# Kernel tuning notes

Hardware: AMD Instinct MI355X
Metric: run time of the kernel (lower is better)

The kernel has to match this reference:

```python
import jax, jax.numpy as jnp
import numpy as np

B, N, D, TOP_K = 4, 4096, 256, 64
EPS = 1e-12  # F.normalize default eps


def setup_inputs() -> dict:
    key = jax.random.key(0)
    kx, kw, kb = jax.random.split(key, 3)
    x = jax.random.normal(kx, (B, N, D), dtype=jnp.float32)
    # value_fc: nn.Linear(in_dims, in_dims) -> weight [D, D], bias [D]
    lim = 1.0 / np.sqrt(D)
    W = jax.random.uniform(kw, (D, D), dtype=jnp.float32, minval=-lim, maxval=lim)
    b = jax.random.uniform(kb, (D,), dtype=jnp.float32, minval=-lim, maxval=lim)
    return {"x": x, "W": W, "b": b}


def reference(x, W, b):
    # value = value_fc(x)
    value = jnp.einsum("bnd,ed->bne", x, W) + b  # torch Linear: x @ W.T + b
    # F.normalize(x, p=2, dim=-1)
    norm = jnp.linalg.norm(x, axis=-1, keepdims=True)
    normed_x = x / jnp.maximum(norm, EPS)
    # full cosine-similarity matrix [B, N, N]
    cos_sim = jnp.einsum("bnd,bmd->bnm", normed_x, normed_x)
    # topk along last dim, scatter back into zeros
    topk_vals, topk_inds = jax.lax.top_k(cos_sim, TOP_K)  # [B, N, K]
    b_idx = jnp.arange(x.shape[0])[:, None, None]
    n_idx = jnp.arange(x.shape[1])[None, :, None]
    attn_sparse = jnp.zeros_like(cos_sim).at[b_idx, n_idx, topk_inds].set(topk_vals)
    # softmax over full row (zeros at non-topk positions contribute exp(0))
    attn = jax.nn.softmax(attn_sparse, axis=-1)
    return jnp.einsum("bnm,bmd->bnd", attn, value)
```

## Files before the change

kernel.cpp:

```cpp
#include <hip/hip_runtime.h>
#include <hip/hip_bf16.h>
#include <stdint.h>

#define B_ 4
#define N_ 4096
#define D_ 256
#define K_ 64
#define BN_ (B_*N_)

typedef __attribute__((ext_vector_type(8))) short bf16x8;
typedef __attribute__((ext_vector_type(8))) unsigned short u16x8;
typedef __attribute__((ext_vector_type(4))) float f32x4;
typedef __attribute__((address_space(1))) const unsigned int gas_u32;
typedef __attribute__((address_space(3))) unsigned int las_u32;

static __device__ __forceinline__ unsigned short f2bf(float f) {
  union { float f; unsigned u; } x; x.f = f;
  unsigned r = x.u + 0x7fffu + ((x.u >> 16) & 1u);
  return (unsigned short)(r >> 16);
}
static __device__ __forceinline__ float bf2f(unsigned short u) {
  union { unsigned u; float f; } x; x.u = ((unsigned)u) << 16;
  return x.f;
}
static __device__ __forceinline__ f32x4 mfma16(bf16x8 a, bf16x8 b, f32x4 c) {
  return __builtin_amdgcn_mfma_f32_16x16x32_bf16(a, b, c, 0, 0, 0);
}

__global__ __launch_bounds__(256) void prep_kernel(
    const float* __restrict__ x, const float* __restrict__ W,
    unsigned short* __restrict__ xn, float* __restrict__ norms,
    unsigned short* __restrict__ Wb, float* __restrict__ vsum) {
  const int bid = blockIdx.x;
  if (bid < 4096) {
    int row = bid * 4 + (threadIdx.x >> 6);
    int lane = threadIdx.x & 63;
    const float4 v = reinterpret_cast<const float4*>(x + (size_t)row * D_)[lane];
    float ss = v.x*v.x + v.y*v.y + v.z*v.z + v.w*v.w;
    #pragma unroll
    for (int off = 32; off > 0; off >>= 1) ss += __shfl_xor(ss, off);
    float nrm = sqrtf(ss);
    float scale = 1.0f / fmaxf(nrm, 1e-12f);
    ushort4 o;
    o.x = f2bf(v.x * scale); o.y = f2bf(v.y * scale);
    o.z = f2bf(v.z * scale); o.w = f2bf(v.w * scale);
    reinterpret_cast<ushort4*>(xn + (size_t)row * D_)[lane] = o;
    if (lane == 0) norms[row] = nrm;
  } else if (bid < 4160) {
    int i = (bid - 4096) * 256 + threadIdx.x;
    float4 v = reinterpret_cast<const float4*>(W)[i];
    ushort4 o; o.x = f2bf(v.x); o.y = f2bf(v.y); o.z = f2bf(v.z); o.w = f2bf(v.w);
    reinterpret_cast<ushort4*>(Wb)[i] = o;
  } else {
    reinterpret_cast<float4*>(vsum)[threadIdx.x] = (float4){0.f, 0.f, 0.f, 0.f};
  }
}

__global__ __launch_bounds__(256, 3) void compute_kernel(
    const unsigned short* __restrict__ xn, const float* __restrict__ norms,
    const unsigned short* __restrict__ Wb, const float* __restrict__ bias,
    unsigned short* __restrict__ value, float* __restrict__ vsum,
    unsigned short* __restrict__ S) {
  __shared__ __attribute__((aligned(16))) unsigned char smem[33792];
  unsigned char* As = smem;
  unsigned char* Bs = smem + 16384;
  float* ns_s   = (float*)(smem + 32768);
  float* bias_s = (float*)(smem + 33280);

  const int t = threadIdx.x, lane = t & 63, w = t >> 6;
  const int l15 = lane & 15, qv = lane >> 4, rb = qv * 4;
  const int wr = w >> 1, wc = w & 1;
  const int x7 = l15 & 7;

  const unsigned short* Asrc;
  const unsigned short* Bsrc;
  int rbG, cb, batch = 0;
  const bool vmode = (blockIdx.x < 256);
  if (vmode) {
    rbG = (blockIdx.x >> 1) * 128;
    cb  = (blockIdx.x & 1) * 128;
    Asrc = xn + (size_t)rbG * D_;
    Bsrc = Wb + (size_t)cb * D_;
    if (t < 128) { ns_s[t] = norms[rbG + t]; bias_s[t] = bias[cb + t]; }
  } else {
    int g = blockIdx.x - 256;
    batch = g >> 10;
    int tl = g & 1023;
    rbG = (tl >> 5) * 128;
    cb  = (tl & 31) * 128;
    Asrc = xn + ((size_t)batch * N_ + rbG) * D_;
    Bsrc = xn + ((size_t)batch * N_ + cb)  * D_;
  }

  auto STAGE = [&](int kk) {
    #pragma unroll
    for (int p = 0; p < 4; p++) {
      int q = t + p * 256;
      int row = q >> 3, c = q & 7;
      int cg = (c ^ (row & 7)) * 8;
      __builtin_amdgcn_global_load_lds(
          (gas_u32*)(Asrc + (size_t)row * D_ + kk * 64 + cg),
          (las_u32*)(As + q * 16), 16, 0, 0);
      __builtin_amdgcn_global_load_lds(
          (gas_u32*)(Bsrc + (size_t)row * D_ + kk * 64 + cg),
          (las_u32*)(Bs + q * 16), 16, 0, 0);
    }
  };

  f32x4 acc[4][4];
  #pragma unroll
  for (int i = 0; i < 4; i++)
    #pragma unroll
    for (int j = 0; j < 4; j++) acc[i][j] = (f32x4){0.f,0.f,0.f,0.f};

  STAGE(0);
  __syncthreads();
  for (int kk = 0; kk < 4; kk++) {
    bf16x8 afr[2][4], bfr[2][4];
    #pragma unroll
    for (int ks = 0; ks < 2; ks++) {
      const int cpos = (((ks * 4 + qv) ^ x7) << 4);
      #pragma unroll
      for (int rt = 0; rt < 4; rt++)
        afr[ks][rt] = *(const bf16x8*)(As + (wr*64 + rt*16 + l15) * 128 + cpos);
      #pragma unroll
      for (int ct = 0; ct < 4; ct++)
        bfr[ks][ct] = *(const bf16x8*)(Bs + (wc*64 + ct*16 + l15) * 128 + cpos);
    }
    __syncthreads();
    if (kk < 3) STAGE(kk + 1);
    #pragma unroll
    for (int ks = 0; ks < 2; ks++)
      #pragma unroll
      for (int rt = 0; rt < 4; rt++)
        #pragma unroll
        for (int ct = 0; ct < 4; ct++)
          acc[rt][ct] = mfma16(afr[ks][rt], bfr[ks][ct], acc[rt][ct]);
    if (kk < 3) __syncthreads();
  }

  unsigned short* kbuf = (unsigned short*)smem;
  if (vmode) {
    float vpart[4] = {0.f, 0.f, 0.f, 0.f};
    #pragma unroll
    for (int rt = 0; rt < 4; rt++)
      #pragma unroll
      for (int ct = 0; ct < 4; ct++) {
        int col_l = wc*64 + ct*16 + l15;
        #pragma unroll
        for (int reg = 0; reg < 4; reg++) {
          int row_l = wr*64 + rt*16 + rb + reg;
          float v = acc[rt][ct][reg] * ns_s[row_l] + bias_s[col_l];
          int pos = (col_l & 7) | ((((col_l >> 3) ^ (row_l & 7))) << 3);
          kbuf[row_l * 128 + pos] = f2bf(v);
          vpart[ct] += v;
        }
      }
    int b2 = rbG >> 12;
    #pragma unroll
    for (int ct = 0; ct < 4; ct++)
      atomicAdd(&vsum[b2*D_ + cb + wc*64 + ct*16 + l15], vpart[ct]);
    __syncthreads();
    #pragma unroll
    for (int p = 0; p < 8; p++) {
      int q = t + p * 256;
      int row = q >> 4, c8 = q & 15;
      u16x8 d = *(const u16x8*)(kbuf + row * 128 + ((c8 ^ (row & 7)) << 3));
      *(u16x8*)(value + (size_t)(rbG + row) * D_ + cb + c8 * 8) = d;
    }
  } else {
    #pragma unroll
    for (int rt = 0; rt < 4; rt++)
      #pragma unroll
      for (int ct = 0; ct < 4; ct++) {
        int col_l = wc*64 + ct*16 + l15;
        #pragma unroll
        for (int reg = 0; reg < 4; reg++) {
          int row_l = wr*64 + rt*16 + rb + reg;
          unsigned short bits = f2bf(acc[rt][ct][reg]);
          unsigned short key = (bits & 0x8000u) ? (unsigned short)(~bits)
                                                : (unsigned short)(bits | 0x8000u);
          int pos = (col_l & 7) | ((((col_l >> 3) ^ (row_l & 7))) << 3);
          kbuf[row_l * 128 + pos] = key;
        }
      }
    __syncthreads();
    unsigned short* Sb = S + ((size_t)batch << 24);
    #pragma unroll
    for (int p = 0; p < 8; p++) {
      int q = t + p * 256;
      int row = q >> 4, c8 = q & 15;
      u16x8 d = *(const u16x8*)(kbuf + row * 128 + ((c8 ^ (row & 7)) << 3));
      *(u16x8*)(Sb + (size_t)(rbG + row) * N_ + cb + c8 * 8) = d;
    }
  }
}

__global__ __launch_bounds__(256) void select_kernel(
    const unsigned short* __restrict__ S,
    const unsigned short* __restrict__ value,
    const float* __restrict__ vsum,
    float* __restrict__ out) {
  __shared__ unsigned hist[4][1024];
  __shared__ unsigned pair2[4][64][2];
  __shared__ int cnts[4][2];

  const int t = threadIdx.x, lane = t & 63, w = t >> 6;
  const int rowg = blockIdx.x * 4 + w;
  const int b = rowg >> 12;
  const int r = rowg & 4095;
  const unsigned short* srow = S + ((size_t)b << 24) + ((size_t)r << 12);

  uint4 kq[8];
  #pragma unroll
  for (int c = 0; c < 8; c++)
    kq[c] = *(const uint4*)(srow + c*512 + lane*8);

  #pragma unroll
  for (int p = 0; p < 4; p++)
    *(uint4*)&hist[w][lane*16 + p*4] = (uint4){0u,0u,0u,0u};
  if (lane == 0) { cnts[w][0] = 0; cnts[w][1] = 0; }

  #pragma unroll
  for (int c = 0; c < 8; c++) {
    unsigned uu[4] = {kq[c].x, kq[c].y, kq[c].z, kq[c].w};
    #pragma unroll
    for (int m = 0; m < 4; m++) {
      unsigned u = uu[m];
      atomicAdd(&hist[w][(u & 0xffffu) >> 6], 1u << (((u >> 5) & 1u) * 16));
      atomicAdd(&hist[w][u >> 22],            1u << (((u >> 21) & 1u) * 16));
    }
  }

  unsigned hw[16];
  #pragma unroll
  for (int p = 0; p < 4; p++)
    *(uint4*)&hw[p*4] = *(const uint4*)&hist[w][lane*16 + p*4];
  unsigned ltot = 0;
  #pragma unroll
  for (int i = 0; i < 16; i++) ltot += (hw[i] & 0xffffu) + (hw[i] >> 16);

  unsigned v = ltot;
  #pragma unroll
  for (int off = 1; off < 64; off <<= 1) {
    unsigned o = __shfl_down(v, off);
    if (lane + off < 64) v += o;
  }
  unsigned above = v - ltot;
  int pk = -1;
  if (v >= 64u && above < 64u) {
    unsigned c = above; int hbl = 0; unsigned cgl = 0;
    #pragma unroll
    for (int j = 31; j >= 0; j--) {
      unsigned cj = (j & 1) ? (hw[j >> 1] >> 16) : (hw[j >> 1] & 0xffffu);
      unsigned cn = c + cj;
      if (cn >= 64u && c < 64u) { hbl = lane*32 + j; cgl = c; }
      c = cn;
    }
    pk = (hbl << 6) | (int)cgl;
  }
  #pragma unroll
  for (int off = 1; off < 64; off <<= 1) pk = max(pk, __shfl_xor(pk, off));
  const unsigned hb = (unsigned)(pk >> 6);
  const unsigned need2 = 64u - (unsigned)(pk & 63);

  if (lane < 16) hist[w][lane] = 0;
  #pragma unroll
  for (int c = 0; c < 8; c++) {
    unsigned uu[4] = {kq[c].x, kq[c].y, kq[c].z, kq[c].w};
    #pragma unroll
    for (int m = 0; m < 4; m++) {
      unsigned klo = uu[m] & 0xffffu, khi = uu[m] >> 16;
      if ((klo >> 5) == hb) atomicAdd(&hist[w][(klo & 31u) >> 1], 1u << ((klo & 1u) * 16));
      if ((khi >> 5) == hb) atomicAdd(&hist[w][(khi & 31u) >> 1], 1u << ((khi & 1u) * 16));
    }
  }
  unsigned wv2 = hist[w][lane >> 1];
  unsigned c2 = (lane & 1) ? (wv2 >> 16) : (wv2 & 0xffffu);
  unsigned s2 = c2;
  #pragma unroll
  for (int off = 1; off < 32; off <<= 1) {
    unsigned o = __shfl_down(s2, off);
    if (lane + off < 32) s2 += o;
  }
  unsigned ab2 = s2 - c2;
  int pk2 = -1;
  if (lane < 32 && s2 >= need2 && ab2 < need2) pk2 = (lane << 6) | (int)ab2;
  #pragma unroll
  for (int off = 1; off < 64; off <<= 1) pk2 = max(pk2, __shfl_xor(pk2, off));
  const unsigned tau = (hb << 5) | (unsigned)(pk2 >> 6);
  const int needeq = (int)need2 - (pk2 & 63);

  float zloc = 0.f;
  #pragma unroll
  for (int c = 0; c < 8; c++) {
    int cb0 = c*512 + lane*8;
    unsigned uu[4] = {kq[c].x, kq[c].y, kq[c].z, kq[c].w};
    #pragma unroll
    for (int m = 0; m < 4; m++) {
      #pragma unroll
      for (int h = 0; h < 2; h++) {
        unsigned key = h ? (uu[m] >> 16) : (uu[m] & 0xffffu);
        bool take = key > tau;
        if (!take && key == tau) { int k = atomicAdd(&cnts[w][1], 1); take = (k < needeq); }
        if (take) {
          int slot = atomicAdd(&cnts[w][0], 1);
          unsigned short bits = (key & 0x8000u) ? (unsigned short)(key & 0x7fffu)
                                                : (unsigned short)(~key);
          float e = __expf(bf2f(bits));
          zloc += e;
          pair2[w][slot][0] = (unsigned)(cb0 + m*2 + h) << 9;
          pair2[w][slot][1] = __float_as_uint(e - 1.0f);
        }
      }
    }
  }
  #pragma unroll
  for (int off = 32; off > 0; off >>= 1) zloc += __shfl_xor(zloc, off);
  const float invZ = 1.0f / (zloc + (float)(N_ - K_));

  const char* vbb = (const char*)value + ((size_t)b << 21);
  float a0 = 0.f, a1 = 0.f, a2 = 0.f, a3 = 0.f;
  for (int i = 0; i < 64; i++) {
    uint2 pr = *(const uint2*)&pair2[w][i][0];
    float wt = __uint_as_float(pr.y);
    uint2 vv = *(const uint2*)(vbb + pr.x + lane*8);
    a0 += wt * __uint_as_float(vv.x << 16);
    a1 += wt * __uint_as_float(vv.x & 0xffff0000u);
    a2 += wt * __uint_as_float(vv.y << 16);
    a3 += wt * __uint_as_float(vv.y & 0xffff0000u);
  }
  float4 vs = *(const float4*)(vsum + b*D_ + lane*4);
  float4 o;
  o.x = (a0 + vs.x) * invZ; o.y = (a1 + vs.y) * invZ;
  o.z = (a2 + vs.z) * invZ; o.w = (a3 + vs.w) * invZ;
  *(float4*)(out + (size_t)rowg * D_ + lane*4) = o;
}

extern "C" void kernel_launch(void* const* d_in, const int* in_sizes, int n_in,
                              void* d_out, int out_size, void* d_ws, size_t ws_size,
                              hipStream_t stream) {
  const float* x    = (const float*)d_in[0];
  const float* W    = (const float*)d_in[1];
  const float* bias = (const float*)d_in[2];
  float* out = (float*)d_out;
  char* ws = (char*)d_ws;
  unsigned short* xn    = (unsigned short*)(ws);
  unsigned short* Wb    = (unsigned short*)(ws + 8388608);
  float*          norms = (float*)(ws + 8519680);
  unsigned short* value = (unsigned short*)(ws + 8585216);
  float*          vsum  = (float*)(ws + 16973824);
  unsigned short* S     = (unsigned short*)(ws + 16977920);

  prep_kernel<<<4161, 256, 0, stream>>>(x, W, xn, norms, Wb, vsum);
  compute_kernel<<<4352, 256, 0, stream>>>(xn, norms, Wb, bias, value, vsum, S);
  select_kernel<<<BN_/4, 256, 0, stream>>>(S, value, vsum, out);
}
```

Before: 211.7 us.

## Remap block order and streamline top-k threshold selection with ballots and bitmasks

Blocks are remapped through a strided index so value-projection and similarity tiles are interleaved across the grid instead of running in blockIdx order. The top-k radix select now finds the histogram bucket with ballot/ffs plus a 32-lane scan in place of a serial per-lane loop and max-reductions. It skips the second histogram pass when the whole boundary bucket fits. Selection builds per-lane bitmasks of keys above and equal to the threshold and loops only over set bits, re-reading keys from shared memory. This reduces divergent per-element branches and atomics, at the cost of extra shared-memory reads and more complex control flow.

```diff
diff --git a/kernel.cpp b/kernel.cpp
--- a/kernel.cpp
+++ b/kernel.cpp
@@ -72,18 +72,20 @@
   const int wr = w >> 1, wc = w & 1;
   const int x7 = l15 & 7;
 
+  const int bidx = (blockIdx.x & 7) * 544 + (blockIdx.x >> 3);
+
   const unsigned short* Asrc;
   const unsigned short* Bsrc;
   int rbG, cb, batch = 0;
-  const bool vmode = (blockIdx.x < 256);
+  const bool vmode = (bidx < 256);
   if (vmode) {
-    rbG = (blockIdx.x >> 1) * 128;
-    cb  = (blockIdx.x & 1) * 128;
+    rbG = (bidx >> 1) * 128;
+    cb  = (bidx & 1) * 128;
     Asrc = xn + (size_t)rbG * D_;
     Bsrc = Wb + (size_t)cb * D_;
     if (t < 128) { ns_s[t] = norms[rbG + t]; bias_s[t] = bias[cb + t]; }
   } else {
-    int g = blockIdx.x - 256;
+    int g = bidx - 256;
     batch = g >> 10;
     int tl = g & 1023;
     rbG = (tl >> 5) * 128;
@@ -247,72 +249,99 @@
     if (lane + off < 64) v += o;
   }
   unsigned above = v - ltot;
-  int pk = -1;
-  if (v >= 64u && above < 64u) {
-    unsigned c = above; int hbl = 0; unsigned cgl = 0;
-    #pragma unroll
-    for (int j = 31; j >= 0; j--) {
-      unsigned cj = (j & 1) ? (hw[j >> 1] >> 16) : (hw[j >> 1] & 0xffffu);
-      unsigned cn = c + cj;
-      if (cn >= 64u && c < 64u) { hbl = lane*32 + j; cgl = c; }
-      c = cn;
-    }
-    pk = (hbl << 6) | (int)cgl;
-  }
-  #pragma unroll
-  for (int off = 1; off < 64; off <<= 1) pk = max(pk, __shfl_xor(pk, off));
-  const unsigned hb = (unsigned)(pk >> 6);
-  const unsigned need2 = 64u - (unsigned)(pk & 63);
-
-  if (lane < 16) hist[w][lane] = 0;
+  unsigned long long m1 = __ballot(v >= 64u && above < 64u);
+  int bl = (int)(__ffsll(m1) - 1);
+  unsigned above_bl = __shfl(above, bl);
+
+  unsigned wbc = hist[w][bl*16 + ((lane & 31) >> 1)];
+  unsigned cj = (lane & 1) ? (wbc >> 16) : (wbc & 0xffffu);
+  unsigned sv = cj;
+  #pragma unroll
+  for (int off = 1; off < 32; off <<= 1) {
+    unsigned o = __shfl_down(sv, off);
+    if (lane + off < 32) sv += o;
+  }
+  unsigned sj = sv + above_bl;
+  unsigned abj = sj - cj;
+  unsigned long long m2 = __ballot(lane < 32 && sj >= 64u && abj < 64u);
+  int jb = (int)(__ffsll(m2) - 1);
+  const unsigned hb = ((unsigned)bl << 5) | (unsigned)jb;
+  const unsigned cg = __shfl(abj, jb);
+  const unsigned cjc = __shfl(cj, jb);
+  const unsigned need2 = 64u - cg;
+
+  unsigned tau; int needeq;
+  if (need2 == cjc && hb > 0u) {
+    tau = (hb << 5) - 1u; needeq = 0;
+  } else {
+    if (lane < 16) hist[w][lane] = 0;
+    #pragma unroll
+    for (int c = 0; c < 8; c++) {
+      unsigned uu[4] = {kq[c].x, kq[c].y, kq[c].z, kq[c].w};
+      #pragma unroll
+      for (int m = 0; m < 4; m++) {
+        unsigned klo = uu[m] & 0xffffu, khi = uu[m] >> 16;
+        if ((klo >> 5) == hb) atomicAdd(&hist[w][(klo & 31u) >> 1], 1u << ((klo & 1u) * 16));
+        if ((khi >> 5) == hb) atomicAdd(&hist[w][(khi & 31u) >> 1], 1u << ((khi & 1u) * 16));
+      }
+    }
+    unsigned wv2 = hist[w][(lane & 31) >> 1];
+    unsigned c2 = (lane & 1) ? (wv2 >> 16) : (wv2 & 0xffffu);
+    unsigned s2 = c2;
+    #pragma unroll
+    for (int off = 1; off < 32; off <<= 1) {
+      unsigned o = __shfl_down(s2, off);
+      if (lane + off < 32) s2 += o;
+    }
+    unsigned ab2 = s2 - c2;
+    unsigned long long m3 = __ballot(lane < 32 && s2 >= need2 && ab2 < need2);
+    int lb = (int)(__ffsll(m3) - 1);
+    unsigned cg2 = __shfl(ab2, lb);
+    tau = (hb << 5) | (unsigned)lb;
+    needeq = (int)(need2 - cg2);
+  }
+
+  float zloc = 0.f;
+  unsigned long long gtm = 0ull, eqm = 0ull;
   #pragma unroll
   for (int c = 0; c < 8; c++) {
     unsigned uu[4] = {kq[c].x, kq[c].y, kq[c].z, kq[c].w};
     #pragma unroll
     for (int m = 0; m < 4; m++) {
       unsigned klo = uu[m] & 0xffffu, khi = uu[m] >> 16;
-      if ((klo >> 5) == hb) atomicAdd(&hist[w][(klo & 31u) >> 1], 1u << ((klo & 1u) * 16));
-      if ((khi >> 5) == hb) atomicAdd(&hist[w][(khi & 31u) >> 1], 1u << ((khi & 1u) * 16));
-    }
-  }
-  unsigned wv2 = hist[w][lane >> 1];
-  unsigned c2 = (lane & 1) ? (wv2 >> 16) : (wv2 & 0xffffu);
-  unsigned s2 = c2;
-  #pragma unroll
-  for (int off = 1; off < 32; off <<= 1) {
-    unsigned o = __shfl_down(s2, off);
-    if (lane + off < 32) s2 += o;
-  }
-  unsigned ab2 = s2 - c2;
-  int pk2 = -1;
-  if (lane < 32 && s2 >= need2 && ab2 < need2) pk2 = (lane << 6) | (int)ab2;
-  #pragma unroll
-  for (int off = 1; off < 64; off <<= 1) pk2 = max(pk2, __shfl_xor(pk2, off));
-  const unsigned tau = (hb << 5) | (unsigned)(pk2 >> 6);
-  const int needeq = (int)need2 - (pk2 & 63);
-
-  float zloc = 0.f;
-  #pragma unroll
-  for (int c = 0; c < 8; c++) {
-    int cb0 = c*512 + lane*8;
-    unsigned uu[4] = {kq[c].x, kq[c].y, kq[c].z, kq[c].w};
-    #pragma unroll
-    for (int m = 0; m < 4; m++) {
-      #pragma unroll
-      for (int h = 0; h < 2; h++) {
-        unsigned key = h ? (uu[m] >> 16) : (uu[m] & 0xffffu);
-        bool take = key > tau;
-        if (!take && key == tau) { int k = atomicAdd(&cnts[w][1], 1); take = (k < needeq); }
-        if (take) {
-          int slot = atomicAdd(&cnts[w][0], 1);
-          unsigned short bits = (key & 0x8000u) ? (unsigned short)(key & 0x7fffu)
-                                                : (unsigned short)(~key);
-          float e = __expf(bf2f(bits));
-          zloc += e;
-          pair2[w][slot][0] = (unsigned)(cb0 + m*2 + h) << 9;
-          pair2[w][slot][1] = __float_as_uint(e - 1.0f);
-        }
-      }
+      int base = c*8 + m*2;
+      gtm |= ((unsigned long long)(klo > tau)) << base;
+      gtm |= ((unsigned long long)(khi > tau)) << (base + 1);
+      eqm |= ((unsigned long long)(klo == tau)) << base;
+      eqm |= ((unsigned long long)(khi == tau)) << (base + 1);
+    }
+  }
+  while (gtm) {
+    int i = (int)(__ffsll(gtm) - 1); gtm &= gtm - 1ull;
+    int col = (i >> 3) * 512 + lane * 8 + (i & 7);
+    unsigned key = srow[col];
+    unsigned short bits = (key & 0x8000u) ? (unsigned short)(key & 0x7fffu)
+                                          : (unsigned short)(~key);
+    float e = __expf(bf2f(bits));
+    zloc += e;
+    int slot = atomicAdd(&cnts[w][0], 1);
+    pair2[w][slot][0] = (unsigned)col << 9;
+    pair2[w][slot][1] = __float_as_uint(e - 1.0f);
+  }
+  if (needeq > 0 && eqm) {
+    unsigned short bitsq = (tau & 0x8000u) ? (unsigned short)(tau & 0x7fffu)
+                                           : (unsigned short)(~tau);
+    float etau = __expf(bf2f(bitsq));
+    float em1 = etau - 1.0f;
+    while (eqm) {
+      int i = (int)(__ffsll(eqm) - 1); eqm &= eqm - 1ull;
+      int k = atomicAdd(&cnts[w][1], 1);
+      if (k >= needeq) break;
+      int col = (i >> 3) * 512 + lane * 8 + (i & 7);
+      zloc += etau;
+      int slot = atomicAdd(&cnts[w][0], 1);
+      pair2[w][slot][0] = (unsigned)col << 9;
+      pair2[w][slot][1] = __float_as_uint(em1);
     }
   }
   #pragma unroll
```

After: 249.4 us. 1.18x slower.

## Raise compute-kernel occupancy and split select histograms per half-wave

Applied to the files above, without the earlier changes.

The compute kernel drops its small shared-memory arrays for norms and bias and loads those values straight into registers. This trims LDS to 32 KB and raises the launch-bounds occupancy hint from 3 to 4 blocks. The select kernel gives each half-wave its own histogram copy, aimed at reducing LDS atomic contention, and sums the two copies when reading. The cost is doubled histogram shared memory in select, tighter register limits in compute, and extra global loads in the value epilogue.

```diff
diff --git a/kernel.cpp b/kernel.cpp
--- a/kernel.cpp
+++ b/kernel.cpp
@@ -56,34 +56,33 @@
   }
 }
 
-__global__ __launch_bounds__(256, 3) void compute_kernel(
+__global__ __launch_bounds__(256, 4) void compute_kernel(
     const unsigned short* __restrict__ xn, const float* __restrict__ norms,
     const unsigned short* __restrict__ Wb, const float* __restrict__ bias,
     unsigned short* __restrict__ value, float* __restrict__ vsum,
     unsigned short* __restrict__ S) {
-  __shared__ __attribute__((aligned(16))) unsigned char smem[33792];
+  __shared__ __attribute__((aligned(16))) unsigned char smem[32768];
   unsigned char* As = smem;
   unsigned char* Bs = smem + 16384;
-  float* ns_s   = (float*)(smem + 32768);
-  float* bias_s = (float*)(smem + 33280);
 
   const int t = threadIdx.x, lane = t & 63, w = t >> 6;
   const int l15 = lane & 15, qv = lane >> 4, rb = qv * 4;
   const int wr = w >> 1, wc = w & 1;
   const int x7 = l15 & 7;
 
+  const int bidx = blockIdx.x;
+
   const unsigned short* Asrc;
   const unsigned short* Bsrc;
   int rbG, cb, batch = 0;
-  const bool vmode = (blockIdx.x < 256);
+  const bool vmode = (bidx < 256);
   if (vmode) {
-    rbG = (blockIdx.x >> 1) * 128;
-    cb  = (blockIdx.x & 1) * 128;
+    rbG = (bidx >> 1) * 128;
+    cb  = (bidx & 1) * 128;
     Asrc = xn + (size_t)rbG * D_;
     Bsrc = Wb + (size_t)cb * D_;
-    if (t < 128) { ns_s[t] = norms[rbG + t]; bias_s[t] = bias[cb + t]; }
   } else {
-    int g = blockIdx.x - 256;
+    int g = bidx - 256;
     batch = g >> 10;
     int tl = g & 1023;
     rbG = (tl >> 5) * 128;
@@ -141,6 +140,15 @@
 
   unsigned short* kbuf = (unsigned short*)smem;
   if (vmode) {
+    float nsv[4][4], bsv[4];
+    #pragma unroll
+    for (int rt = 0; rt < 4; rt++)
+      #pragma unroll
+      for (int reg = 0; reg < 4; reg++)
+        nsv[rt][reg] = norms[rbG + wr*64 + rt*16 + rb + reg];
+    #pragma unroll
+    for (int ct = 0; ct < 4; ct++)
+      bsv[ct] = bias[cb + wc*64 + ct*16 + l15];
     float vpart[4] = {0.f, 0.f, 0.f, 0.f};
     #pragma unroll
     for (int rt = 0; rt < 4; rt++)
@@ -150,7 +158,7 @@
         #pragma unroll
         for (int reg = 0; reg < 4; reg++) {
           int row_l = wr*64 + rt*16 + rb + reg;
-          float v = acc[rt][ct][reg] * ns_s[row_l] + bias_s[col_l];
+          float v = acc[rt][ct][reg] * nsv[rt][reg] + bsv[ct];
           int pos = (col_l & 7) | ((((col_l >> 3) ^ (row_l & 7))) << 3);
           kbuf[row_l * 128 + pos] = f2bf(v);
           vpart[ct] += v;
@@ -201,11 +209,12 @@
     const unsigned short* __restrict__ value,
     const float* __restrict__ vsum,
     float* __restrict__ out) {
-  __shared__ unsigned hist[4][1024];
+  __shared__ unsigned hist2[8][1024];
   __shared__ unsigned pair2[4][64][2];
   __shared__ int cnts[4][2];
 
   const int t = threadIdx.x, lane = t & 63, w = t >> 6;
+  const int cpi = w*2 + (lane >> 5);
   const int rowg = blockIdx.x * 4 + w;
   const int b = rowg >> 12;
   const int r = rowg & 4095;
@@ -216,9 +225,12 @@
   for (int c = 0; c < 8; c++)
     kq[c] = *(const uint4*)(srow + c*512 + lane*8);
 
-  #pragma unroll
-  for (int p = 0; p < 4; p++)
-    *(uint4*)&hist[w][lane*16 + p*4] = (uint4){0u,0u,0u,0u};
+  {
+    unsigned* hb0 = &hist2[w*2][0];
+    #pragma unroll
+    for (int p = 0; p < 8; p++)
+      *(uint4*)&hb0[lane*32 + p*4] = (uint4){0u,0u,0u,0u};
+  }
   if (lane == 0) { cnts[w][0] = 0; cnts[w][1] = 0; }
 
   #pragma unroll
@@ -227,15 +239,19 @@
     #pragma unroll
     for (int m = 0; m < 4; m++) {
       unsigned u = uu[m];
-      atomicAdd(&hist[w][(u & 0xffffu) >> 6], 1u << (((u >> 5) & 1u) * 16));
-      atomicAdd(&hist[w][u >> 22],            1u << (((u >> 21) & 1u) * 16));
+      atomicAdd(&hist2[cpi][(u & 0xffffu) >> 6], 1u << (((u >> 5) & 1u) * 16));
+      atomicAdd(&hist2[cpi][u >> 22],            1u << (((u >> 21) & 1u) * 16));
     }
   }
 
   unsigned hw[16];
   #pragma unroll
-  for (int p = 0; p < 4; p++)
-    *(uint4*)&hw[p*4] = *(const uint4*)&hist[w][lane*16 + p*4];
+  for (int p = 0; p < 4; p++) {
+    uint4 A0 = *(const uint4*)&hist2[w*2][lane*16 + p*4];
+    uint4 A1 = *(const uint4*)&hist2[w*2+1][lane*16 + p*4];
+    hw[p*4+0] = A0.x + A1.x; hw[p*4+1] = A0.y + A1.y;
+    hw[p*4+2] = A0.z + A1.z; hw[p*4+3] = A0.w + A1.w;
+  }
   unsigned ltot = 0;
   #pragma unroll
   for (int i = 0; i < 16; i++) ltot += (hw[i] & 0xffffu) + (hw[i] >> 16);
@@ -264,18 +280,18 @@
   const unsigned hb = (unsigned)(pk >> 6);
   const unsigned need2 = 64u - (unsigned)(pk & 63);
 
-  if (lane < 16) hist[w][lane] = 0;
+  if (lane < 32) hist2[w*2 + (lane >> 4)][lane & 15] = 0;
   #pragma unroll
   for (int c = 0; c < 8; c++) {
     unsigned uu[4] = {kq[c].x, kq[c].y, kq[c].z, kq[c].w};
     #pragma unroll
     for (int m = 0; m < 4; m++) {
       unsigned klo = uu[m] & 0xffffu, khi = uu[m] >> 16;
-      if ((klo >> 5) == hb) atomicAdd(&hist[w][(klo & 31u) >> 1], 1u << ((klo & 1u) * 16));
-      if ((khi >> 5) == hb) atomicAdd(&hist[w][(khi & 31u) >> 1], 1u << ((khi & 1u) * 16));
-    }
-  }
-  unsigned wv2 = hist[w][lane >> 1];
+      if ((klo >> 5) == hb) atomicAdd(&hist2[cpi][(klo & 31u) >> 1], 1u << ((klo & 1u) * 16));
+      if ((khi >> 5) == hb) atomicAdd(&hist2[cpi][(khi & 31u) >> 1], 1u << ((khi & 1u) * 16));
+    }
+  }
+  unsigned wv2 = hist2[w*2][(lane & 31) >> 1] + hist2[w*2+1][(lane & 31) >> 1];
   unsigned c2 = (lane & 1) ? (wv2 >> 16) : (wv2 & 0xffffu);
   unsigned s2 = c2;
   #pragma unroll
```

Result: slower. 241.8 us (+14.2%).

## Double-buffer LDS staging in compute kernel and load norms/bias into registers

Applied to the files above, without the earlier changes.

Doubles shared memory to 64KB so the next K-slice is staged into a second buffer while the current one is consumed. This removes one of the two barriers per K-iteration. Norm and bias values for the value epilogue are now read straight from global memory into registers instead of through shared memory. The larger LDS footprint lowers launch bounds from 3 to 2 blocks per CU, so latency hiding across blocks drops in exchange for overlap within each block.

```diff
diff --git a/kernel.cpp b/kernel.cpp
--- a/kernel.cpp
+++ b/kernel.cpp
@@ -56,34 +56,31 @@
   }
 }
 
-__global__ __launch_bounds__(256, 3) void compute_kernel(
+__global__ __launch_bounds__(256, 2) void compute_kernel(
     const unsigned short* __restrict__ xn, const float* __restrict__ norms,
     const unsigned short* __restrict__ Wb, const float* __restrict__ bias,
     unsigned short* __restrict__ value, float* __restrict__ vsum,
     unsigned short* __restrict__ S) {
-  __shared__ __attribute__((aligned(16))) unsigned char smem[33792];
-  unsigned char* As = smem;
-  unsigned char* Bs = smem + 16384;
-  float* ns_s   = (float*)(smem + 32768);
-  float* bias_s = (float*)(smem + 33280);
+  __shared__ __attribute__((aligned(16))) unsigned char smem[65536];
 
   const int t = threadIdx.x, lane = t & 63, w = t >> 6;
   const int l15 = lane & 15, qv = lane >> 4, rb = qv * 4;
   const int wr = w >> 1, wc = w & 1;
   const int x7 = l15 & 7;
 
+  const int bidx = blockIdx.x;
+
   const unsigned short* Asrc;
   const unsigned short* Bsrc;
   int rbG, cb, batch = 0;
-  const bool vmode = (blockIdx.x < 256);
+  const bool vmode = (bidx < 256);
   if (vmode) {
-    rbG = (blockIdx.x >> 1) * 128;
-    cb  = (blockIdx.x & 1) * 128;
+    rbG = (bidx >> 1) * 128;
+    cb  = (bidx & 1) * 128;
     Asrc = xn + (size_t)rbG * D_;
     Bsrc = Wb + (size_t)cb * D_;
-    if (t < 128) { ns_s[t] = norms[rbG + t]; bias_s[t] = bias[cb + t]; }
   } else {
-    int g = blockIdx.x - 256;
+    int g = bidx - 256;
     batch = g >> 10;
     int tl = g & 1023;
     rbG = (tl >> 5) * 128;
@@ -92,7 +89,7 @@
     Bsrc = xn + ((size_t)batch * N_ + cb)  * D_;
   }
 
-  auto STAGE = [&](int kk) {
+  auto STAGE = [&](int kk, unsigned char* Ad, unsigned char* Bd) {
     #pragma unroll
     for (int p = 0; p < 4; p++) {
       int q = t + p * 256;
@@ -100,10 +97,10 @@
       int cg = (c ^ (row & 7)) * 8;
       __builtin_amdgcn_global_load_lds(
           (gas_u32*)(Asrc + (size_t)row * D_ + kk * 64 + cg),
-          (las_u32*)(As + q * 16), 16, 0, 0);
+          (las_u32*)(Ad + q * 16), 16, 0, 0);
       __builtin_amdgcn_global_load_lds(
           (gas_u32*)(Bsrc + (size_t)row * D_ + kk * 64 + cg),
-          (las_u32*)(Bs + q * 16), 16, 0, 0);
+          (las_u32*)(Bd + q * 16), 16, 0, 0);
     }
   };
 
@@ -113,22 +110,27 @@
     #pragma unroll
     for (int j = 0; j < 4; j++) acc[i][j] = (f32x4){0.f,0.f,0.f,0.f};
 
-  STAGE(0);
+  STAGE(0, smem, smem + 16384);
   __syncthreads();
+  int cur = 0;
   for (int kk = 0; kk < 4; kk++) {
+    unsigned char* Ac = smem + cur * 32768;
+    unsigned char* Bc = Ac + 16384;
+    if (kk < 3) {
+      unsigned char* An = smem + (cur ^ 1) * 32768;
+      STAGE(kk + 1, An, An + 16384);
+    }
     bf16x8 afr[2][4], bfr[2][4];
     #pragma unroll
     for (int ks = 0; ks < 2; ks++) {
       const int cpos = (((ks * 4 + qv) ^ x7) << 4);
       #pragma unroll
       for (int rt = 0; rt < 4; rt++)
-        afr[ks][rt] = *(const bf16x8*)(As + (wr*64 + rt*16 + l15) * 128 + cpos);
+        afr[ks][rt] = *(const bf16x8*)(Ac + (wr*64 + rt*16 + l15) * 128 + cpos);
       #pragma unroll
       for (int ct = 0; ct < 4; ct++)
-        bfr[ks][ct] = *(const bf16x8*)(Bs + (wc*64 + ct*16 + l15) * 128 + cpos);
-    }
-    __syncthreads();
-    if (kk < 3) STAGE(kk + 1);
+        bfr[ks][ct] = *(const bf16x8*)(Bc + (wc*64 + ct*16 + l15) * 128 + cpos);
+    }
     #pragma unroll
     for (int ks = 0; ks < 2; ks++)
       #pragma unroll
@@ -136,11 +138,21 @@
         #pragma unroll
         for (int ct = 0; ct < 4; ct++)
           acc[rt][ct] = mfma16(afr[ks][rt], bfr[ks][ct], acc[rt][ct]);
-    if (kk < 3) __syncthreads();
+    __syncthreads();
+    cur ^= 1;
   }
 
   unsigned short* kbuf = (unsigned short*)smem;
   if (vmode) {
+    float nsv[4][4], bsv[4];
+    #pragma unroll
+    for (int rt = 0; rt < 4; rt++)
+      #pragma unroll
+      for (int reg = 0; reg < 4; reg++)
+        nsv[rt][reg] = norms[rbG + wr*64 + rt*16 + rb + reg];
+    #pragma unroll
+    for (int ct = 0; ct < 4; ct++)
+      bsv[ct] = bias[cb + wc*64 + ct*16 + l15];
     float vpart[4] = {0.f, 0.f, 0.f, 0.f};
     #pragma unroll
     for (int rt = 0; rt < 4; rt++)
@@ -150,7 +162,7 @@
         #pragma unroll
         for (int reg = 0; reg < 4; reg++) {
           int row_l = wr*64 + rt*16 + rb + reg;
-          float v = acc[rt][ct][reg] * ns_s[row_l] + bias_s[col_l];
+          float v = acc[rt][ct][reg] * nsv[rt][reg] + bsv[ct];
           int pos = (col_l & 7) | ((((col_l >> 3) ^ (row_l & 7))) << 3);
           kbuf[row_l * 128 + pos] = f2bf(v);
           vpart[ct] += v;
```

Measured after the change: 221.7 us. 4.7% more time.
